# Optimization experiments

Measured on AMD Instinct MI355X. Metric: run time of the kernel, lower is better.

The kernel has to match this reference:

```python
import jax, jax.numpy as jnp
import numpy as np

B, I, O, C = 8192, 256, 256, 32


def setup_inputs() -> dict:
    key = jax.random.key(0)
    k1, k2, k3, k4 = jax.random.split(key, 4)
    x = jax.random.normal(k1, (B, I), dtype=jnp.float32)
    idx_channel = jax.random.randint(k2, (B,), 0, C, dtype=jnp.int64)
    # learned params per init_kwargs: weight [O, I, C], bias [O, C]
    weight = jax.random.normal(k3, (O, I, C), dtype=jnp.float32) * (1.0 / np.sqrt(I))
    bias = jax.random.normal(k4, (O, C), dtype=jnp.float32) * (1.0 / np.sqrt(O))
    return {"x": x, "idx_channel": idx_channel, "weight": weight, "bias": bias}


def reference(x, idx_channel, weight, bias):
    # Original: one_hot(idx) @ weight then batched matvec; mathematically this is
    # a per-sample gather of weight[..., idx[b]] followed by a batched GEMV + bias.
    w_sel = jnp.take(weight, idx_channel, axis=2)          # [O, I, B]
    b_sel = jnp.take(bias, idx_channel, axis=1).T          # [B, O]
    out = jnp.einsum('oib,bi->bo', w_sel, x) + b_sel       # [B, O]
    return out
```

## Files before the change

### kernel.cpp

```cpp
#include <hip/hip_runtime.h>
#include <hip/hip_bf16.h>

#define NB 8192
#define NI 256
#define NO 256
#define NC 32

typedef __attribute__((ext_vector_type(8))) short short8;
typedef __attribute__((ext_vector_type(4))) float floatx4;

#define WS_COUNTS_OFF 0
#define WS_LISTS_OFF  (4u << 10)
#define WS_WT_OFF     (1u << 20)

static __device__ __forceinline__ unsigned short f2bf(float f) {
    __hip_bfloat16 h = __float2bfloat16(f);
    return *(unsigned short*)&h;
}

#define PREP_BLOCKS 288

__global__ __launch_bounds__(256) void k_prep(
        const int* __restrict__ idx,
        const float* __restrict__ w,
        unsigned int* __restrict__ counts,
        unsigned short* __restrict__ lists,
        unsigned short* __restrict__ wT) {
    const int bid = blockIdx.x;
    const int tid = threadIdx.x;

    if (bid < 256) {
        int g = bid * 256 + tid;
        const float4* src = (const float4*)(w + (size_t)g * NC);
        unsigned short vals[NC];
#pragma unroll
        for (int s = 0; s < 8; ++s) {
            float4 v = src[s];
            vals[s * 4 + 0] = f2bf(v.x);
            vals[s * 4 + 1] = f2bf(v.y);
            vals[s * 4 + 2] = f2bf(v.z);
            vals[s * 4 + 3] = f2bf(v.w);
        }
#pragma unroll
        for (int c = 0; c < NC; ++c) {
            wT[(size_t)c * (NO * NI) + g] = vals[c];
        }
    } else {
        __shared__ unsigned int lcnt;
        const int c = bid - 256;
        if (tid == 0) lcnt = 0u;
        __syncthreads();
        const int4* idx4 = (const int4*)idx;
        for (int t = tid; t < NB / 4; t += 256) {
            int4 v = idx4[t];
            int b0 = t * 4;
            if (v.x == c) lists[c * NB + atomicAdd(&lcnt, 1u)] = (unsigned short)(b0 + 0);
            if (v.y == c) lists[c * NB + atomicAdd(&lcnt, 1u)] = (unsigned short)(b0 + 1);
            if (v.z == c) lists[c * NB + atomicAdd(&lcnt, 1u)] = (unsigned short)(b0 + 2);
            if (v.w == c) lists[c * NB + atomicAdd(&lcnt, 1u)] = (unsigned short)(b0 + 3);
        }
        __syncthreads();
        if (tid == 0) counts[c] = lcnt;
    }
}

__launch_bounds__(256)
__global__ void k_gemm(const float* __restrict__ x,
                       const unsigned short* __restrict__ wT,
                       const float* __restrict__ bias,
                       const unsigned int* __restrict__ counts,
                       const unsigned short* __restrict__ lists,
                       float* __restrict__ out) {
    const int c  = blockIdx.x;
    const int o0 = blockIdx.y * 64;
    const int cnt = (int)counts[c];

    __shared__ unsigned short As[64][136];
    __shared__ unsigned short Bs[64][136];
    __shared__ int blist[64];

    const int tid  = threadIdx.x;
    const int wv   = tid >> 6;
    const int lane = tid & 63;
    const int lrc  = lane & 15;
    const int koff = (lane >> 4) * 8;
    const int rbase = (lane >> 4) * 4;

    const unsigned short* wTc = wT + ((size_t)c * NO + o0) * NI;
    const int o = o0 + wv * 16 + lrc;
    const float bv = bias[o * NC + c];

    for (int mt = blockIdx.z; mt * 64 < cnt; mt += 8) {
        const int m0 = mt * 64;
        if (tid < 64) {
            int mr = m0 + tid;
            blist[tid] = (int)lists[c * NB + (mr < cnt ? mr : m0)];
        }
        __syncthreads();

        floatx4 acc[4];
#pragma unroll
        for (int ms = 0; ms < 4; ++ms) acc[ms] = (floatx4){0.f, 0.f, 0.f, 0.f};

#pragma unroll
        for (int kt = 0; kt < 2; ++kt) {
            const int kb = kt * 128;
#pragma unroll
            for (int s = 0; s < 4; ++s) {
                int lin = tid + s * 256;
                int row = lin >> 4;
                int c8  = (lin & 15) * 8;
                const float4* pa = (const float4*)(x + (size_t)blist[row] * NI + kb + c8);
                float4 a0 = pa[0], a1 = pa[1];
                unsigned short r[8];
                r[0] = f2bf(a0.x); r[1] = f2bf(a0.y); r[2] = f2bf(a0.z); r[3] = f2bf(a0.w);
                r[4] = f2bf(a1.x); r[5] = f2bf(a1.y); r[6] = f2bf(a1.z); r[7] = f2bf(a1.w);
                *(uint4*)&As[row][c8] = *(uint4*)r;
                *(uint4*)&Bs[row][c8] = *(const uint4*)(wTc + (size_t)row * NI + kb + c8);
            }
            __syncthreads();

            const int n0 = wv * 16;
#pragma unroll
            for (int k0 = 0; k0 < 4; ++k0) {
                short8 bfrag = *(const short8*)&Bs[n0 + lrc][k0 * 32 + koff];
#pragma unroll
                for (int ms = 0; ms < 4; ++ms) {
                    short8 afrag = *(const short8*)&As[ms * 16 + lrc][k0 * 32 + koff];
                    acc[ms] = __builtin_amdgcn_mfma_f32_16x16x32_bf16(afrag, bfrag, acc[ms], 0, 0, 0);
                }
            }
            __syncthreads();
        }

#pragma unroll
        for (int ms = 0; ms < 4; ++ms) {
#pragma unroll
            for (int r = 0; r < 4; ++r) {
                int row = ms * 16 + rbase + r;
                if (m0 + row < cnt) {
                    out[(size_t)blist[row] * NO + o] = acc[ms][r] + bv;
                }
            }
        }
        __syncthreads();
    }
}

extern "C" void kernel_launch(void* const* d_in, const int* in_sizes, int n_in,
                              void* d_out, int out_size, void* d_ws, size_t ws_size,
                              hipStream_t stream) {
    const float* x    = (const float*)d_in[0];
    const int*   idx  = (const int*)d_in[1];
    const float* w    = (const float*)d_in[2];
    const float* bias = (const float*)d_in[3];
    float* out = (float*)d_out;

    char* ws = (char*)d_ws;
    unsigned int*   counts = (unsigned int*)(ws + WS_COUNTS_OFF);
    unsigned short* lists  = (unsigned short*)(ws + WS_LISTS_OFF);
    unsigned short* wT     = (unsigned short*)(ws + WS_WT_OFF);

    k_prep<<<PREP_BLOCKS, 256, 0, stream>>>(idx, w, counts, lists, wT);
    dim3 grid(NC, NO / 64, 8);
    k_gemm<<<grid, 256, 0, stream>>>(x, wT, bias, counts, lists, out);
}
```

Before: 83.17 us.

## Fuse prep and GEMM kernels into one launch with a flag-based grid barrier

Merges the weight-transpose/bucket-building kernel and the grouped GEMM into a single 512-block kernel. Blocks that finish prep work publish a flag (or count+1) in the workspace, and every block spins on all 288 flags before starting its GEMM tile. This removes the second launch and the gap between kernels, and cuts the z-split of the GEMM grid from 8 to 4. In exchange it relies on all 512 blocks being co-resident to avoid deadlock, and on the workspace flags being reset to zero or the poison value before each call; otherwise later calls could read stale flags and race ahead of the prep work.

Measured after the change: 104.4 us. +25.5%, slower.

```diff
diff --git a/kernel.cpp b/kernel.cpp
--- a/kernel.cpp
+++ b/kernel.cpp
@@ -6,10 +6,13 @@
 #define NO 256
 #define NC 32
 
+#define POISON 0xAAAAAAAAu
+#define NFLAGS 288
+
 typedef __attribute__((ext_vector_type(8))) short short8;
 typedef __attribute__((ext_vector_type(4))) float floatx4;
 
-#define WS_COUNTS_OFF 0
+#define WS_FLAGS_OFF  0
 #define WS_LISTS_OFF  (4u << 10)
 #define WS_WT_OFF     (1u << 20)
 
@@ -18,14 +21,20 @@
     return *(unsigned short*)&h;
 }
 
-#define PREP_BLOCKS 288
+__global__ __launch_bounds__(256) void k_fused(
+        const int* __restrict__ idx,
+        const float* __restrict__ x,
+        const float* __restrict__ w,
+        const float* __restrict__ bias,
+        unsigned int* flags,
+        unsigned short* __restrict__ lists,
+        unsigned short* __restrict__ wT,
+        float* __restrict__ out) {
+    __shared__ unsigned short As[64][136];
+    __shared__ unsigned short Bs[64][136];
+    __shared__ int blist[64];
+    __shared__ unsigned int lcnt;
 
-__global__ __launch_bounds__(256) void k_prep(
-        const int* __restrict__ idx,
-        const float* __restrict__ w,
-        unsigned int* __restrict__ counts,
-        unsigned short* __restrict__ lists,
-        unsigned short* __restrict__ wT) {
     const int bid = blockIdx.x;
     const int tid = threadIdx.x;
 
@@ -45,8 +54,12 @@
         for (int c = 0; c < NC; ++c) {
             wT[(size_t)c * (NO * NI) + g] = vals[c];
         }
-    } else {
-        __shared__ unsigned int lcnt;
+        __syncthreads();
+        if (tid == 0) {
+            __threadfence();
+            atomicExch(&flags[bid], 1u);
+        }
+    } else if (bid < 288) {
         const int c = bid - 256;
         if (tid == 0) lcnt = 0u;
         __syncthreads();
@@ -60,37 +73,45 @@
             if (v.w == c) lists[c * NB + atomicAdd(&lcnt, 1u)] = (unsigned short)(b0 + 3);
         }
         __syncthreads();
-        if (tid == 0) counts[c] = lcnt;
+        if (tid == 0) {
+            __threadfence();
+            atomicExch(&flags[bid], lcnt + 1u);
+        }
     }
-}
 
-__launch_bounds__(256)
-__global__ void k_gemm(const float* __restrict__ x,
-                       const unsigned short* __restrict__ wT,
-                       const float* __restrict__ bias,
-                       const unsigned int* __restrict__ counts,
-                       const unsigned short* __restrict__ lists,
-                       float* __restrict__ out) {
-    const int c  = blockIdx.x;
-    const int o0 = blockIdx.y * 64;
-    const int cnt = (int)counts[c];
+    if (tid < 64) {
+        bool done = false;
+        while (!done) {
+            unsigned int miss = 0u;
+#pragma unroll
+            for (int f = tid; f < NFLAGS; f += 64) {
+                unsigned int v = atomicAdd(&flags[f], 0u);
+                miss |= (unsigned int)(v == POISON || v == 0u);
+            }
+            done = (__ballot(miss != 0u) == 0ull);
+            if (!done) __builtin_amdgcn_s_sleep(2);
+        }
+        if (tid == 0) __threadfence();
+    }
+    __syncthreads();
 
-    __shared__ unsigned short As[64][136];
-    __shared__ unsigned short Bs[64][136];
-    __shared__ int blist[64];
+    const int c    = bid & 31;
+    const int rest = bid >> 5;
+    const int o0   = (rest & 3) * 64;
+    const int z    = rest >> 2;
+    const int cnt  = (int)(flags[256 + c] - 1u);
 
-    const int tid  = threadIdx.x;
-    const int wv   = tid >> 6;
-    const int lane = tid & 63;
-    const int lrc  = lane & 15;
-    const int koff = (lane >> 4) * 8;
+    const int wv    = tid >> 6;
+    const int lane  = tid & 63;
+    const int lrc   = lane & 15;
+    const int koff  = (lane >> 4) * 8;
     const int rbase = (lane >> 4) * 4;
 
     const unsigned short* wTc = wT + ((size_t)c * NO + o0) * NI;
     const int o = o0 + wv * 16 + lrc;
     const float bv = bias[o * NC + c];
 
-    for (int mt = blockIdx.z; mt * 64 < cnt; mt += 8) {
+    for (int mt = z; mt * 64 < cnt; mt += 4) {
         const int m0 = mt * 64;
         if (tid < 64) {
             int mr = m0 + tid;
@@ -157,11 +178,9 @@
     float* out = (float*)d_out;
 
     char* ws = (char*)d_ws;
-    unsigned int*   counts = (unsigned int*)(ws + WS_COUNTS_OFF);
-    unsigned short* lists  = (unsigned short*)(ws + WS_LISTS_OFF);
-    unsigned short* wT     = (unsigned short*)(ws + WS_WT_OFF);
+    unsigned int*   flags = (unsigned int*)(ws + WS_FLAGS_OFF);
+    unsigned short* lists = (unsigned short*)(ws + WS_LISTS_OFF);
+    unsigned short* wT    = (unsigned short*)(ws + WS_WT_OFF);
 
-    k_prep<<<PREP_BLOCKS, 256, 0, stream>>>(idx, w, counts, lists, wT);
-    dim3 grid(NC, NO / 64, 8);
-    k_gemm<<<grid, 256, 0, stream>>>(x, wT, bias, counts, lists, out);
+    k_fused<<<512, 256, 0, stream>>>(idx, x, w, bias, flags, lists, wT, out);
 }
```

## Drop LDS staging in grouped GEMM; keep weight fragments in registers, load x directly

Applied to the files above, without the earlier changes.

The GEMM kernel no longer stages x and weight tiles through shared memory. Each wave loads its 16-column weight fragment for the full K=256 into registers once per block and reuses it across all row tiles. Each lane reads its x rows straight from global memory into MFMA A fragments, which removes every __syncthreads and the LDS traffic. Blocks with no rows exit early, and launch bounds now request 4 blocks per CU. In exchange, x is read with strided per-lane 32-byte loads, and the extra registers may cut occupancy.

After: 101.0 us. 21.4% more time.

```diff
diff --git a/kernel.cpp b/kernel.cpp
--- a/kernel.cpp
+++ b/kernel.cpp
@@ -64,73 +64,62 @@
     }
 }
 
-__launch_bounds__(256)
-__global__ void k_gemm(const float* __restrict__ x,
-                       const unsigned short* __restrict__ wT,
-                       const float* __restrict__ bias,
-                       const unsigned int* __restrict__ counts,
-                       const unsigned short* __restrict__ lists,
-                       float* __restrict__ out) {
-    const int c  = blockIdx.x;
-    const int o0 = blockIdx.y * 64;
+__global__ __launch_bounds__(256, 4) void k_gemm(
+        const float* __restrict__ x,
+        const unsigned short* __restrict__ wT,
+        const float* __restrict__ bias,
+        const unsigned int* __restrict__ counts,
+        const unsigned short* __restrict__ lists,
+        float* __restrict__ out) {
+    const int c   = blockIdx.x;
+    const int o0  = blockIdx.y * 64;
     const int cnt = (int)counts[c];
-
-    __shared__ unsigned short As[64][136];
-    __shared__ unsigned short Bs[64][136];
-    __shared__ int blist[64];
+    if ((int)blockIdx.z * 64 >= cnt) return;
 
     const int tid  = threadIdx.x;
     const int wv   = tid >> 6;
     const int lane = tid & 63;
     const int lrc  = lane & 15;
-    const int koff = (lane >> 4) * 8;
-    const int rbase = (lane >> 4) * 4;
+    const int kg   = lane >> 4;
+    const int koff = kg * 8;
+    const int rbase = kg * 4;
 
-    const unsigned short* wTc = wT + ((size_t)c * NO + o0) * NI;
+    const unsigned short* bp =
+        wT + ((size_t)c * NO + o0 + wv * 16 + lrc) * NI + koff;
+    short8 bq[8];
+#pragma unroll
+    for (int kc = 0; kc < 8; ++kc) bq[kc] = *(const short8*)(bp + kc * 32);
+
     const int o = o0 + wv * 16 + lrc;
     const float bv = bias[o * NC + c];
+    const unsigned short* lc = lists + c * NB;
 
     for (int mt = blockIdx.z; mt * 64 < cnt; mt += 8) {
         const int m0 = mt * 64;
-        if (tid < 64) {
-            int mr = m0 + tid;
-            blist[tid] = (int)lists[c * NB + (mr < cnt ? mr : m0)];
+
+        const float* rp[4];
+#pragma unroll
+        for (int ms = 0; ms < 4; ++ms) {
+            int mr = m0 + ms * 16 + lrc;
+            rp[ms] = x + (size_t)lc[mr < cnt ? mr : m0] * NI + koff;
         }
-        __syncthreads();
 
         floatx4 acc[4];
 #pragma unroll
         for (int ms = 0; ms < 4; ++ms) acc[ms] = (floatx4){0.f, 0.f, 0.f, 0.f};
 
 #pragma unroll
-        for (int kt = 0; kt < 2; ++kt) {
-            const int kb = kt * 128;
+        for (int kc = 0; kc < 8; ++kc) {
 #pragma unroll
-            for (int s = 0; s < 4; ++s) {
-                int lin = tid + s * 256;
-                int row = lin >> 4;
-                int c8  = (lin & 15) * 8;
-                const float4* pa = (const float4*)(x + (size_t)blist[row] * NI + kb + c8);
-                float4 a0 = pa[0], a1 = pa[1];
+            for (int ms = 0; ms < 4; ++ms) {
+                float4 a0 = *(const float4*)(rp[ms] + kc * 32);
+                float4 a1 = *(const float4*)(rp[ms] + kc * 32 + 4);
                 unsigned short r[8];
                 r[0] = f2bf(a0.x); r[1] = f2bf(a0.y); r[2] = f2bf(a0.z); r[3] = f2bf(a0.w);
                 r[4] = f2bf(a1.x); r[5] = f2bf(a1.y); r[6] = f2bf(a1.z); r[7] = f2bf(a1.w);
-                *(uint4*)&As[row][c8] = *(uint4*)r;
-                *(uint4*)&Bs[row][c8] = *(const uint4*)(wTc + (size_t)row * NI + kb + c8);
+                acc[ms] = __builtin_amdgcn_mfma_f32_16x16x32_bf16(
+                    *(const short8*)r, bq[kc], acc[ms], 0, 0, 0);
             }
-            __syncthreads();
-
-            const int n0 = wv * 16;
-#pragma unroll
-            for (int k0 = 0; k0 < 4; ++k0) {
-                short8 bfrag = *(const short8*)&Bs[n0 + lrc][k0 * 32 + koff];
-#pragma unroll
-                for (int ms = 0; ms < 4; ++ms) {
-                    short8 afrag = *(const short8*)&As[ms * 16 + lrc][k0 * 32 + koff];
-                    acc[ms] = __builtin_amdgcn_mfma_f32_16x16x32_bf16(afrag, bfrag, acc[ms], 0, 0, 0);
-                }
-            }
-            __syncthreads();
         }
 
 #pragma unroll
@@ -139,11 +128,10 @@
             for (int r = 0; r < 4; ++r) {
                 int row = ms * 16 + rbase + r;
                 if (m0 + row < cnt) {
-                    out[(size_t)blist[row] * NO + o] = acc[ms][r] + bv;
+                    out[(size_t)lc[m0 + row] * NO + o] = acc[ms][r] + bv;
                 }
             }
         }
-        __syncthreads();
     }
 }
 
```
